# Kernel tuning notes

Measured on AMD Instinct MI355X. Metric: run time of the kernel, lower is better.

## Reference

```python
import jax, jax.numpy as jnp
import numpy as np

N = 100000      # nodes
E = 1000000     # edges
IN = 512
H = [512, 256]
C = 64          # n_classes
K = 10          # propagation steps
ALPHA = 0.1


def _glorot(key, shape):
    lim = np.sqrt(6.0 / (shape[0] + shape[1])).astype(np.float32)
    return jax.random.uniform(key, shape, jnp.float32, -lim, lim)


def setup_inputs() -> dict:
    key = jax.random.key(0)
    ks = jax.random.split(key, 6)
    features = jax.random.normal(ks[0], (N, IN), jnp.float32)
    edge_index = jax.random.randint(ks[1], (2, E), 0, N)  # int32/64 src,dst
    W0 = _glorot(ks[2], (H[0], IN)); b0 = jnp.zeros((H[0],), jnp.float32)
    W1 = _glorot(ks[3], (H[1], H[0])); b1 = jnp.zeros((H[1],), jnp.float32)
    W2 = _glorot(ks[4], (C, H[1])); b2 = jnp.zeros((C,), jnp.float32)
    return dict(features=features, edge_index=edge_index,
                W0=W0, b0=b0, W1=W1, b1=b1, W2=W2, b2=b2)


def _appnp(h, src, dst):
    # DGL APPNPConv: symmetric normalization D_out^{-1/2} A D_in^{-1/2},
    # degrees clamped to min 1; h_{t+1} = (1-a) * norm_agg + a * h_0.
    ones = jnp.ones(src.shape, h.dtype)
    deg_out = jax.ops.segment_sum(ones, src, num_segments=N)
    deg_in = jax.ops.segment_sum(ones, dst, num_segments=N)
    norm_src = jnp.maximum(deg_out, 1.0) ** -0.5  # [N]
    norm_dst = jnp.maximum(deg_in, 1.0) ** -0.5   # [N]
    h0 = h
    for _ in range(K):
        msg = (h * norm_src[:, None])[src]                     # [E, C] gather
        agg = jax.ops.segment_sum(msg, dst, num_segments=N)    # [N, C] scatter-add
        h = (1.0 - ALPHA) * agg * norm_dst[:, None] + ALPHA * h0
    return h


def reference(features, edge_index, W0, b0, W1, b1, W2, b2):
    src, dst = edge_index[0], edge_index[1]
    h = jax.nn.relu(features @ W0.T + b0)   # [N, 512]
    h = jax.nn.relu(h @ W1.T + b1)          # [N, 256]
    h = h @ W2.T + b2                       # [N, 64] logits
    return _appnp(h, src, dst)
```

## Files before the change

### kernel.cpp

```cpp
#include <hip/hip_runtime.h>
#include <hip/hip_bf16.h>

#define NN_NODES 100000
#define NE_EDGES 1000000
#define D_IN 512
#define D_H0 512
#define D_H1 256
#define D_C  64

using f32x4  = __attribute__((ext_vector_type(4))) float;
using h16x8  = __attribute__((ext_vector_type(8))) _Float16;

static __device__ __forceinline__ void gll16(const _Float16* g, _Float16* l){
    __builtin_amdgcn_global_load_lds(
        (const __attribute__((address_space(1))) unsigned int*)g,
        (__attribute__((address_space(3))) unsigned int*)l, 16, 0, 0);
}

__global__ __launch_bounds__(256) void tof16_tiled_kernel(
    const float* __restrict__ w, _Float16* __restrict__ o, int R, int K)
{
    int i = blockIdx.x * 256 + threadIdx.x;
    int n8 = R * (K >> 3);
    if (i >= n8) return;
    int kd = K >> 3;
    int r  = i / kd;
    int c0 = (i - r * kd) * 8;
    const f32x4 a = *(const f32x4*)(w + (size_t)r * K + c0);
    const f32x4 b = *(const f32x4*)(w + (size_t)r * K + c0 + 4);
    h16x8 h;
    #pragma unroll
    for (int j = 0; j < 4; j++){
        h[j]   = (_Float16)a[j];
        h[j+4] = (_Float16)b[j];
    }
    size_t off = ((size_t)(r >> 7) * (K >> 5) + (c0 >> 5)) * 4096
               + (size_t)(r & 127) * 32 + (c0 & 31);
    *(h16x8*)(o + off) = h;
}

template<bool RELU, int OMODE, int BN_T, int NBN, int KK>
__global__ __launch_bounds__(256, 4) void gemm_kernel(
    const _Float16* __restrict__ A,
    const _Float16* __restrict__ B,
    const float* __restrict__ bias,
    void* __restrict__ O1, _Float16* __restrict__ O2, const float* __restrict__ scale,
    int M, int NNc, int xq, int xr)
{
    constexpr int NTK  = KK / 32;
    constexpr int NF   = BN_T / 32;
    constexpr int BBLK = BN_T / 16;
    constexpr int TOT  = 8 + BBLK;
    constexpr int LPW  = TOT / 4;

    __shared__ _Float16 sA[2][128 * 32];
    __shared__ _Float16 sB[2][BN_T * 32];

    const int tid  = threadIdx.x;
    const int lane = tid & 63;
    const int wv   = tid >> 6;
    const int wm   = wv >> 1;
    const int wn   = wv & 1;
    const int fr   = lane & 15;
    const int fc   = lane >> 4;

    const int bid = blockIdx.x;
    const int xcd = bid & 7;
    const int i8  = bid >> 3;
    const int L   = ((xcd < xr) ? xcd * (xq + 1) : xr * (xq + 1) + (xcd - xr) * xq) + i8;
    const int mt  = L / NBN;
    const int bn  = L - mt * NBN;
    const int bm0 = mt * 128;
    const int bn0 = bn * BN_T;

    const int bslab = bn0 >> 7;
    const int binsl = bn0 & 127;

    const int loff = (lane >> 2) * 32 + ((lane & 3) ^ ((lane >> 3) & 3)) * 8;

    f32x4 acc[4][NF] = {};

    auto stage = [&](int b, int t){
        const _Float16* as = A + ((size_t)mt * NTK + t) * 4096;
        const _Float16* bs = B + ((size_t)bslab * NTK + t) * 4096 + binsl * 32;
        #pragma unroll
        for (int u = 0; u < LPW; u++){
            int idx = u * 4 + wv;
            if (idx < 8) gll16(as + idx * 512 + loff, sA[b] + idx * 512);
            else         gll16(bs + (idx - 8) * 512 + loff, sB[b] + (idx - 8) * 512);
        }
    };

    auto compute = [&](int b){
        h16x8 bf[NF];
        #pragma unroll
        for (int nf = 0; nf < NF; nf++){
            int r = wn * (BN_T / 2) + nf * 16 + fr;
            int c = (fc ^ ((r >> 1) & 3)) * 8;
            bf[nf] = *(const h16x8*)&sB[b][r * 32 + c];
        }
        h16x8 af[4];
        #pragma unroll
        for (int mf = 0; mf < 4; mf++){
            int r = wm * 64 + mf * 16 + fr;
            int c = (fc ^ ((r >> 1) & 3)) * 8;
            af[mf] = *(const h16x8*)&sA[b][r * 32 + c];
        }
        __builtin_amdgcn_s_setprio(1);
        #pragma unroll
        for (int mf = 0; mf < 4; mf++)
            #pragma unroll
            for (int nf = 0; nf < NF; nf++)
                acc[mf][nf] = __builtin_amdgcn_mfma_f32_16x16x32_f16(af[mf], bf[nf], acc[mf][nf], 0, 0, 0);
        __builtin_amdgcn_s_setprio(0);
    };

    stage(0, 0);
    __syncthreads();
    int cur = 0;
    for (int t = 0; t < NTK; t++){
        if (t + 1 < NTK) stage(cur ^ 1, t + 1);
        compute(cur);
        __syncthreads();
        cur ^= 1;
    }

    #pragma unroll
    for (int mf = 0; mf < 4; mf++){
        #pragma unroll
        for (int nf = 0; nf < NF; nf++){
            #pragma unroll
            for (int r = 0; r < 4; r++){
                int rg = bm0 + wm * 64 + mf * 16 + fc * 4 + r;
                int cg = bn0 + wn * (BN_T / 2) + nf * 16 + fr;
                if (rg < M){
                    float v = acc[mf][nf][r] + bias[cg];
                    if constexpr (RELU) v = fmaxf(v, 0.f);
                    if constexpr (OMODE == 1){
                        size_t o = ((size_t)mt * (NNc >> 5) + (cg >> 5)) * 4096
                                 + (size_t)(rg & 127) * 32 + (cg & 31);
                        ((_Float16*)O1)[o] = (_Float16)v;
                    } else {
                        ((_Float16*)O1)[(size_t)rg * NNc + cg] = (_Float16)v;
                        O2[(size_t)rg * NNc + cg] = (_Float16)(v * scale[rg]);
                    }
                }
            }
        }
    }
}

__global__ __launch_bounds__(512, 2) void gemm23_kernel(
    const _Float16* __restrict__ A,
    const _Float16* __restrict__ B1,
    const _Float16* __restrict__ B2,
    const float* __restrict__ bias1,
    const float* __restrict__ bias2,
    _Float16* __restrict__ h0h, _Float16* __restrict__ h0s,
    const float* __restrict__ nsrc,
    int M, int xq, int xr)
{
    constexpr int NTK = 16;
    __shared__ _Float16 smem[49152];

    const int tid  = threadIdx.x;
    const int lane = tid & 63;
    const int wv   = tid >> 6;
    const int wm   = wv >> 2;
    const int wn   = wv & 3;
    const int fr   = lane & 15;
    const int fc   = lane >> 4;

    const int bid = blockIdx.x;
    const int xcd = bid & 7;
    const int i8  = bid >> 3;
    const int mt  = ((xcd < xr) ? xcd * (xq + 1) : xr * (xq + 1) + (xcd - xr) * xq) + i8;
    const int bm0 = mt * 128;

    const int loff = (lane >> 2) * 32 + ((lane & 3) ^ ((lane >> 3) & 3)) * 8;

    _Float16* sW2 = smem + 32768;

    #pragma unroll
    for (int u = 0; u < 4; u++){
        int idx = u * 8 + wv;
        int k = idx >> 2, rb = idx & 3;
        gll16(B2 + (size_t)k * 4096 + rb * 512 + loff, sW2 + k * 2048 + rb * 512);
    }

    auto sA = [&](int b){ return smem + b * 12288; };
    auto sB = [&](int b){ return smem + b * 12288 + 4096; };

    auto stage = [&](int b, int t){
        #pragma unroll
        for (int u = 0; u < 3; u++){
            int idx = u * 8 + wv;
            if (idx < 8){
                gll16(A + ((size_t)mt * NTK + t) * 4096 + idx * 512 + loff,
                      sA(b) + idx * 512);
            } else {
                int rb = idx - 8;
                gll16(B1 + ((size_t)(rb >> 3) * NTK + t) * 4096 + (rb & 7) * 512 + loff,
                      sB(b) + rb * 512);
            }
        }
    };

    f32x4 acc[4][4] = {};

    auto compute = [&](int b){
        h16x8 bf[4];
        #pragma unroll
        for (int nf = 0; nf < 4; nf++){
            int r = wn * 64 + nf * 16 + fr;
            int c = (fc ^ ((r >> 1) & 3)) * 8;
            bf[nf] = *(const h16x8*)&sB(b)[r * 32 + c];
        }
        h16x8 af[4];
        #pragma unroll
        for (int mf = 0; mf < 4; mf++){
            int r = wm * 64 + mf * 16 + fr;
            int c = (fc ^ ((r >> 1) & 3)) * 8;
            af[mf] = *(const h16x8*)&sA(b)[r * 32 + c];
        }
        __builtin_amdgcn_s_setprio(1);
        #pragma unroll
        for (int mf = 0; mf < 4; mf++)
            #pragma unroll
            for (int nf = 0; nf < 4; nf++)
                acc[mf][nf] = __builtin_amdgcn_mfma_f32_16x16x32_f16(af[mf], bf[nf], acc[mf][nf], 0, 0, 0);
        __builtin_amdgcn_s_setprio(0);
    };

    stage(0, 0);
    __syncthreads();
    int cur = 0;
    for (int t = 0; t < NTK; t++){
        if (t + 1 < NTK) stage(cur ^ 1, t + 1);
        compute(cur);
        __syncthreads();
        cur ^= 1;
    }

    #pragma unroll
    for (int mf = 0; mf < 4; mf++){
        #pragma unroll
        for (int nf = 0; nf < 4; nf++){
            #pragma unroll
            for (int r = 0; r < 4; r++){
                int row = wm * 64 + mf * 16 + fc * 4 + r;
                int col = wn * 64 + nf * 16 + fr;
                float v = fmaxf(acc[mf][nf][r] + bias1[col], 0.f);
                int ci = col & 31;
                int sw = ((ci >> 3) ^ ((row >> 1) & 3)) * 8 + (ci & 7);
                smem[(col >> 5) * 4096 + row * 32 + sw] = (_Float16)v;
            }
        }
    }
    __syncthreads();

    f32x4 acc2[4] = {};
    #pragma unroll
    for (int kk = 0; kk < 8; kk++){
        int ar = wv * 16 + fr;
        int ac = (fc ^ ((ar >> 1) & 3)) * 8;
        h16x8 af = *(const h16x8*)&smem[kk * 4096 + ar * 32 + ac];
        #pragma unroll
        for (int nf = 0; nf < 4; nf++){
            int br = nf * 16 + fr;
            int bc = (fc ^ ((br >> 1) & 3)) * 8;
            h16x8 bf = *(const h16x8*)&sW2[kk * 2048 + br * 32 + bc];
            acc2[nf] = __builtin_amdgcn_mfma_f32_16x16x32_f16(af, bf, acc2[nf], 0, 0, 0);
        }
    }
    #pragma unroll
    for (int nf = 0; nf < 4; nf++){
        #pragma unroll
        for (int r = 0; r < 4; r++){
            int rg = bm0 + wv * 16 + fc * 4 + r;
            int cg = nf * 16 + fr;
            if (rg < M){
                float v = acc2[nf][r] + bias2[cg];
                h0h[(size_t)rg * D_C + cg] = (_Float16)v;
                h0s[(size_t)rg * D_C + cg] = (_Float16)(v * nsrc[rg]);
            }
        }
    }
}

__global__ void degrees_kernel(const int* __restrict__ src, const int* __restrict__ dst,
                               int* __restrict__ dout, int* __restrict__ din){
    int e = blockIdx.x * blockDim.x + threadIdx.x;
    if (e < NE_EDGES){
        atomicAdd(&dout[src[e]], 1);
        atomicAdd(&din[dst[e]], 1);
    }
}

__global__ void norm_kernel(const int* __restrict__ dout, const int* __restrict__ din,
                            float* __restrict__ ns, float* __restrict__ nd, int n){
    int i = blockIdx.x * blockDim.x + threadIdx.x;
    if (i < n){
        ns[i] = rsqrtf((float)(dout[i] > 1 ? dout[i] : 1));
        nd[i] = rsqrtf((float)(din[i]  > 1 ? din[i]  : 1));
    }
}

__global__ __launch_bounds__(256) void scan1_kernel(const int* __restrict__ din,
                                                    int* __restrict__ part,
                                                    int* __restrict__ bsum, int n){
    __shared__ int s[256];
    int i = blockIdx.x * 256 + threadIdx.x;
    int v = (i < n) ? din[i] : 0;
    s[threadIdx.x] = v;
    __syncthreads();
    for (int off = 1; off < 256; off <<= 1){
        int t = (threadIdx.x >= off) ? s[threadIdx.x - off] : 0;
        __syncthreads();
        s[threadIdx.x] += t;
        __syncthreads();
    }
    if (i < n) part[i] = s[threadIdx.x];
    if (threadIdx.x == 255) bsum[blockIdx.x] = s[255];
}

__global__ __launch_bounds__(512) void scan2_kernel(int* __restrict__ bsum, int nb){
    __shared__ int s[512];
    int v = (threadIdx.x < nb) ? bsum[threadIdx.x] : 0;
    s[threadIdx.x] = v;
    __syncthreads();
    for (int off = 1; off < 512; off <<= 1){
        int t = (threadIdx.x >= off) ? s[threadIdx.x - off] : 0;
        __syncthreads();
        s[threadIdx.x] += t;
        __syncthreads();
    }
    if (threadIdx.x < nb) bsum[threadIdx.x] = s[threadIdx.x];
}

__global__ void scan3_kernel(const int* __restrict__ part, const int* __restrict__ din,
                             const int* __restrict__ bsum, int* __restrict__ offs,
                             int* __restrict__ cur, int n){
    int i = blockIdx.x * 256 + threadIdx.x;
    if (i < n){
        int base = (blockIdx.x > 0) ? bsum[blockIdx.x - 1] : 0;
        int excl = base + part[i] - din[i];
        offs[i] = excl;
        cur[i]  = excl;
    }
}

__global__ void fill_kernel(const int* __restrict__ src, const int* __restrict__ dst,
                            int* __restrict__ cur, int* __restrict__ csr){
    int e = blockIdx.x * blockDim.x + threadIdx.x;
    if (e < NE_EDGES){
        int d = dst[e];
        int pos = atomicAdd(&cur[d], 1);
        csr[pos] = src[e];
    }
}

__global__ __launch_bounds__(256) void propagate_kernel(
    const _Float16* __restrict__ hs, const _Float16* __restrict__ h0h,
    float* __restrict__ hout, _Float16* __restrict__ houts,
    const int* __restrict__ offs, const int* __restrict__ din,
    const int* __restrict__ csr,
    const float* __restrict__ ns, const float* __restrict__ nd)
{
    int t    = blockIdx.x * 256 + threadIdx.x;
    int node = t >> 3;
    int gl   = t & 7;
    if (node >= NN_NODES) return;
    int start = offs[node];
    int deg   = din[node];
    float acc[8] = {};
    int j = 0;
    for (; j + 4 <= deg; j += 4){
        int s0 = csr[start + j];
        int s1 = csr[start + j + 1];
        int s2 = csr[start + j + 2];
        int s3 = csr[start + j + 3];
        h16x8 v0 = *(const h16x8*)(hs + (size_t)s0 * D_C + gl * 8);
        h16x8 v1 = *(const h16x8*)(hs + (size_t)s1 * D_C + gl * 8);
        h16x8 v2 = *(const h16x8*)(hs + (size_t)s2 * D_C + gl * 8);
        h16x8 v3 = *(const h16x8*)(hs + (size_t)s3 * D_C + gl * 8);
        #pragma unroll
        for (int i = 0; i < 8; i++)
            acc[i] += ((float)v0[i] + (float)v1[i]) + ((float)v2[i] + (float)v3[i]);
    }
    for (; j < deg; j++){
        int s0 = csr[start + j];
        h16x8 v0 = *(const h16x8*)(hs + (size_t)s0 * D_C + gl * 8);
        #pragma unroll
        for (int i = 0; i < 8; i++) acc[i] += (float)v0[i];
    }
    float ndv = 0.9f * nd[node];
    h16x8 h0v = *(const h16x8*)(h0h + (size_t)node * D_C + gl * 8);
    float out[8];
    #pragma unroll
    for (int i = 0; i < 8; i++) out[i] = acc[i] * ndv + 0.1f * (float)h0v[i];
    if (houts){
        float nsv = ns[node];
        h16x8 o;
        #pragma unroll
        for (int i = 0; i < 8; i++) o[i] = (_Float16)(out[i] * nsv);
        *(h16x8*)(houts + (size_t)node * D_C + gl * 8) = o;
    }
    if (hout){
        f32x4 oa, ob;
        #pragma unroll
        for (int i = 0; i < 4; i++){ oa[i] = out[i]; ob[i] = out[i + 4]; }
        *(f32x4*)(hout + (size_t)node * D_C + gl * 8)     = oa;
        *(f32x4*)(hout + (size_t)node * D_C + gl * 8 + 4) = ob;
    }
}

extern "C" void kernel_launch(void* const* d_in, const int* in_sizes, int n_in,
                              void* d_out, int out_size, void* d_ws, size_t ws_size,
                              hipStream_t stream)
{
    const float* features = (const float*)d_in[0];
    const int*   edge     = (const int*)d_in[1];
    const float* W0 = (const float*)d_in[2];
    const float* b0 = (const float*)d_in[3];
    const float* W1 = (const float*)d_in[4];
    const float* b1 = (const float*)d_in[5];
    const float* W2 = (const float*)d_in[6];
    const float* b2 = (const float*)d_in[7];
    const int* src = edge;
    const int* dst = edge + NE_EDGES;

    char* p = (char*)d_ws;
    auto alloc = [&](size_t bytes) -> char* {
        char* r = p;
        p += (bytes + 255) & ~(size_t)255;
        return r;
    };

    const int MT = (NN_NODES + 127) / 128;
    const size_t FEAT_T = (size_t)MT * 16 * 4096 * 2;
    const size_t HBUFH  = (size_t)NN_NODES * D_C * 2;

    _Float16* w0f = (_Float16*)alloc((size_t)4 * 16 * 4096 * 2);
    _Float16* w1f = (_Float16*)alloc((size_t)2 * 16 * 4096 * 2);
    _Float16* w2f = (_Float16*)alloc((size_t)1 * 8  * 4096 * 2);
    char* R1 = alloc(FEAT_T);
    char* R2 = alloc(FEAT_T);
    int*   deg_out = (int*)alloc((size_t)NN_NODES * 4);
    int*   deg_in  = (int*)alloc((size_t)NN_NODES * 4);
    float* nsrc    = (float*)alloc((size_t)NN_NODES * 4);
    float* ndst    = (float*)alloc((size_t)NN_NODES * 4);
    int*   part    = (int*)alloc((size_t)NN_NODES * 4);
    int*   bsum    = (int*)alloc(2048);
    int*   offs    = (int*)alloc((size_t)NN_NODES * 4);
    int*   cur     = (int*)alloc((size_t)NN_NODES * 4);
    int*   csr     = (int*)alloc((size_t)NE_EDGES * 4);
    if ((size_t)(p - (char*)d_ws) > ws_size) return;

    _Float16* fhf  = (_Float16*)R1;
    _Float16* act1 = (_Float16*)R2;
    _Float16* h0h  = (_Float16*)R1;
    _Float16* h0s  = (_Float16*)(R1 + HBUFH);
    _Float16* hAs  = (_Float16*)(R1 + 2 * HBUFH);
    _Float16* hBs  = (_Float16*)(R1 + 3 * HBUFH);

    hipMemsetAsync(deg_out, 0, (size_t)NN_NODES * 4, stream);
    hipMemsetAsync(deg_in,  0, (size_t)NN_NODES * 4, stream);
    degrees_kernel<<<(NE_EDGES + 255) / 256, 256, 0, stream>>>(src, dst, deg_out, deg_in);
    norm_kernel<<<(NN_NODES + 255) / 256, 256, 0, stream>>>(deg_out, deg_in, nsrc, ndst, NN_NODES);
    int nb = (NN_NODES + 255) / 256;
    scan1_kernel<<<nb, 256, 0, stream>>>(deg_in, part, bsum, NN_NODES);
    scan2_kernel<<<1, 512, 0, stream>>>(bsum, nb);
    scan3_kernel<<<nb, 256, 0, stream>>>(part, deg_in, bsum, offs, cur, NN_NODES);
    fill_kernel<<<(NE_EDGES + 255) / 256, 256, 0, stream>>>(src, dst, cur, csr);

    tof16_tiled_kernel<<<(NN_NODES * D_IN / 8 + 255) / 256, 256, 0, stream>>>(
        features, fhf, NN_NODES, D_IN);
    tof16_tiled_kernel<<<(D_H0 * D_IN / 8 + 255) / 256, 256, 0, stream>>>(W0, w0f, D_H0, D_IN);
    tof16_tiled_kernel<<<(D_H1 * D_H0 / 8 + 255) / 256, 256, 0, stream>>>(W1, w1f, D_H1, D_H0);
    tof16_tiled_kernel<<<(D_C * D_H1 / 8 + 255) / 256, 256, 0, stream>>>(W2, w2f, D_C, D_H1);

    {
        int nwg = MT * 8;
        gemm_kernel<true, 1, 64, 8, 512><<<nwg, 256, 0, stream>>>(
            fhf, w0f, b0, act1, nullptr, nullptr, NN_NODES, D_H0, nwg / 8, nwg % 8);
    }
    {
        int nwg = MT;
        gemm23_kernel<<<nwg, 512, 0, stream>>>(
            act1, w1f, w2f, b1, b2, h0h, h0s, nsrc, NN_NODES, nwg / 8, nwg % 8);
    }

    const _Float16* curs = h0s;
    _Float16* bufss[2] = { hAs, hBs };
    int pb = (NN_NODES * 8 + 255) / 256;
    for (int it = 0; it < 10; it++){
        float*    out  = (it == 9) ? (float*)d_out : nullptr;
        _Float16* outs = (it == 9) ? nullptr       : bufss[it & 1];
        propagate_kernel<<<pb, 256, 0, stream>>>(curs, h0h, out, outs, offs, deg_in, csr, nsrc, ndst);
        curs = outs;
    }
}
```

Before: 609.0 us.

## Sort nodes by in-degree to balance propagate wavefronts

Result: slower. 1.016 ms (+66.8%).

```diff
diff --git a/kernel.cpp b/kernel.cpp
--- a/kernel.cpp
+++ b/kernel.cpp
@@ -360,19 +360,62 @@
     }
 }
 
+__global__ __launch_bounds__(256) void hist_kernel(const int* __restrict__ din,
+                                                   int* __restrict__ hist){
+    __shared__ int h[64];
+    if (threadIdx.x < 64) h[threadIdx.x] = 0;
+    __syncthreads();
+    int i = blockIdx.x * 256 + threadIdx.x;
+    if (i < NN_NODES){
+        int d = din[i]; if (d > 63) d = 63;
+        atomicAdd(&h[d], 1);
+    }
+    __syncthreads();
+    if (threadIdx.x < 64) atomicAdd(&hist[threadIdx.x], h[threadIdx.x]);
+}
+
+__global__ __launch_bounds__(64) void scan64_kernel(const int* __restrict__ hist,
+                                                    int* __restrict__ cursor){
+    __shared__ int s[64];
+    int v = hist[threadIdx.x];
+    s[threadIdx.x] = v;
+    __syncthreads();
+    for (int off = 1; off < 64; off <<= 1){
+        int t = (threadIdx.x >= off) ? s[threadIdx.x - off] : 0;
+        __syncthreads();
+        s[threadIdx.x] += t;
+        __syncthreads();
+    }
+    cursor[threadIdx.x] = s[threadIdx.x] - v;
+}
+
+__global__ void scatter_kernel(const int* __restrict__ din,
+                               int* __restrict__ cursor, int* __restrict__ perm){
+    int i = blockIdx.x * 256 + threadIdx.x;
+    if (i < NN_NODES){
+        int d = din[i]; if (d > 63) d = 63;
+        int pos = atomicAdd(&cursor[d], 1);
+        perm[pos] = i;
+    }
+}
+
 __global__ __launch_bounds__(256) void propagate_kernel(
     const _Float16* __restrict__ hs, const _Float16* __restrict__ h0h,
     float* __restrict__ hout, _Float16* __restrict__ houts,
     const int* __restrict__ offs, const int* __restrict__ din,
-    const int* __restrict__ csr,
+    const int* __restrict__ csr, const int* __restrict__ perm,
     const float* __restrict__ ns, const float* __restrict__ nd)
 {
-    int t    = blockIdx.x * 256 + threadIdx.x;
-    int node = t >> 3;
-    int gl   = t & 7;
-    if (node >= NN_NODES) return;
+    int t   = blockIdx.x * 256 + threadIdx.x;
+    int idx = t >> 3;
+    int gl  = t & 7;
+    if (idx >= NN_NODES) return;
+    int node  = perm[idx];
     int start = offs[node];
     int deg   = din[node];
+    float ndv = 0.9f * nd[node];
+    float nsv = ns[node];
+    h16x8 h0v = *(const h16x8*)(h0h + (size_t)node * D_C + gl * 8);
     float acc[8] = {};
     int j = 0;
     for (; j + 4 <= deg; j += 4){
@@ -394,13 +437,10 @@
         #pragma unroll
         for (int i = 0; i < 8; i++) acc[i] += (float)v0[i];
     }
-    float ndv = 0.9f * nd[node];
-    h16x8 h0v = *(const h16x8*)(h0h + (size_t)node * D_C + gl * 8);
     float out[8];
     #pragma unroll
     for (int i = 0; i < 8; i++) out[i] = acc[i] * ndv + 0.1f * (float)h0v[i];
     if (houts){
-        float nsv = ns[node];
         h16x8 o;
         #pragma unroll
         for (int i = 0; i < 8; i++) o[i] = (_Float16)(out[i] * nsv);
@@ -455,6 +495,9 @@
     int*   offs    = (int*)alloc((size_t)NN_NODES * 4);
     int*   cur     = (int*)alloc((size_t)NN_NODES * 4);
     int*   csr     = (int*)alloc((size_t)NE_EDGES * 4);
+    int*   hist    = (int*)alloc(256);
+    int*   cursor  = (int*)alloc(256);
+    int*   perm    = (int*)alloc((size_t)NN_NODES * 4);
     if ((size_t)(p - (char*)d_ws) > ws_size) return;
 
     _Float16* fhf  = (_Float16*)R1;
@@ -466,6 +509,7 @@
 
     hipMemsetAsync(deg_out, 0, (size_t)NN_NODES * 4, stream);
     hipMemsetAsync(deg_in,  0, (size_t)NN_NODES * 4, stream);
+    hipMemsetAsync(hist,    0, 256, stream);
     degrees_kernel<<<(NE_EDGES + 255) / 256, 256, 0, stream>>>(src, dst, deg_out, deg_in);
     norm_kernel<<<(NN_NODES + 255) / 256, 256, 0, stream>>>(deg_out, deg_in, nsrc, ndst, NN_NODES);
     int nb = (NN_NODES + 255) / 256;
@@ -473,6 +517,9 @@
     scan2_kernel<<<1, 512, 0, stream>>>(bsum, nb);
     scan3_kernel<<<nb, 256, 0, stream>>>(part, deg_in, bsum, offs, cur, NN_NODES);
     fill_kernel<<<(NE_EDGES + 255) / 256, 256, 0, stream>>>(src, dst, cur, csr);
+    hist_kernel<<<nb, 256, 0, stream>>>(deg_in, hist);
+    scan64_kernel<<<1, 64, 0, stream>>>(hist, cursor);
+    scatter_kernel<<<nb, 256, 0, stream>>>(deg_in, cursor, perm);
 
     tof16_tiled_kernel<<<(NN_NODES * D_IN / 8 + 255) / 256, 256, 0, stream>>>(
         features, fhf, NN_NODES, D_IN);
@@ -497,7 +544,7 @@
     for (int it = 0; it < 10; it++){
         float*    out  = (it == 9) ? (float*)d_out : nullptr;
         _Float16* outs = (it == 9) ? nullptr       : bufss[it & 1];
-        propagate_kernel<<<pb, 256, 0, stream>>>(curs, h0h, out, outs, offs, deg_in, csr, nsrc, ndst);
+        propagate_kernel<<<pb, 256, 0, stream>>>(curs, h0h, out, outs, offs, deg_in, csr, perm, nsrc, ndst);
         curs = outs;
     }
 }
```
